# Performance work log

Hardware: AMD Instinct MI355X
Metric: run time of the kernel (lower is better)

The kernel has to match this reference:

```python
import jax, jax.numpy as jnp
import numpy as np

B, N, D, H, C, K = 4096, 64, 128, 256, 8, 3
L = N * D  # latent_dim = num_patches * d_model = 8192
UQ, LQ = 0.9, 0.1


def setup_inputs() -> dict:
    key = jax.random.key(0)
    ks = jax.random.split(key, 6)
    z = jax.random.normal(ks[0], (B, N, D), dtype=jnp.float32)
    q = jax.random.uniform(ks[1], (B,), dtype=jnp.float32)
    ch_ids = jax.random.randint(ks[2], (B,), 0, C, dtype=jnp.int32)
    # Xavier-style init for the 3 expert MLPs (Linear(L,H), Linear(H,L)) + heads Linear(L,1)
    s1 = float(np.sqrt(2.0 / (L + H)))
    s2 = float(np.sqrt(2.0 / (H + L)))
    sh = float(np.sqrt(2.0 / (L + 1)))
    W1 = jax.random.normal(ks[3], (K, L, H), dtype=jnp.float32) * s1
    W2 = jax.random.normal(ks[4], (K, H, L), dtype=jnp.float32) * s2
    Wh = jax.random.normal(ks[5], (K, L), dtype=jnp.float32) * sh
    return dict(z=z, q=q, ch_ids=ch_ids,
                W1=W1, b1=jnp.zeros((K, H), jnp.float32),
                W2=W2, b2=jnp.zeros((K, L), jnp.float32),
                Wh=Wh, bh=jnp.zeros((K,), jnp.float32))


def _channel_thresholds(q, ch_ids):
    """Per-channel sample-adjusted upper/lower quantiles, torch.quantile(..., interpolation='lower')."""
    def one(c):
        mask = ch_ids == c
        n = jnp.sum(mask).astype(jnp.float32)
        s = jnp.sort(jnp.where(mask, q, jnp.inf))  # channel values occupy first n slots
        au = jnp.ceil((n + 1.0) * UQ) / n
        pu = jnp.where(au > 1.0, UQ, au)
        al = jnp.floor((n + 1.0) * LQ) / n
        pl = jnp.where(al < 0.0, LQ, al)
        iu = jnp.floor(pu * (n - 1.0)).astype(jnp.int32)  # 'lower' interpolation index
        il = jnp.floor(pl * (n - 1.0)).astype(jnp.int32)
        return s[iu], s[il]
    return jax.vmap(one)(jnp.arange(C))  # (C,), (C,)


def reference(z, q, ch_ids, W1, b1, W2, b2, Wh, bh):
    uq_th, lq_th = _channel_thresholds(q, ch_ids)
    group = jnp.where(q <= lq_th[ch_ids], 2,
                      jnp.where(q >= uq_th[ch_ids], 0, 1)).astype(jnp.int32)  # (B,)
    zf = z.reshape(z.shape[0], -1)  # (B, L) -- Flatten(start_dim=-2)

    def expert(w1, c1, w2, c2, wh, ch):
        h = jax.nn.gelu(zf @ w1 + c1, approximate=False)   # (B, H)
        o = h @ w2 + c2                                     # (B, L)
        return o @ wh + ch                                  # (B,)

    logits_all = jax.vmap(expert)(W1, b1, W2, b2, Wh, bh)   # (K, B)
    logits = jnp.take_along_axis(logits_all, group[None, :], axis=0)[0]  # (B,)

    # per-channel softmax over logits (stable), matching torch.softmax on each channel's indices
    m = jax.ops.segment_max(logits, ch_ids, num_segments=C)
    e = jnp.exp(logits - m[ch_ids])
    ssum = jax.ops.segment_sum(e, ch_ids, num_segments=C)
    qwa_coeff = e / ssum[ch_ids]
    refined_probs = q * qwa_coeff
    return refined_probs
```

## Files before the change

kernel.cpp:

```cpp
#include <hip/hip_runtime.h>

typedef unsigned short u16;
typedef unsigned int u32;
typedef __attribute__((ext_vector_type(8))) short short8;
typedef __attribute__((ext_vector_type(4))) float f32x4;

#define NB 4096
#define LDIM 8192
#define HDIM 256
#define NEXP 3
#define NCH 8
#define BK 32

__device__ inline u16 f2bf(float f) {
  u32 u = __float_as_uint(f);
  u += 0x7FFFu + ((u >> 16) & 1u);
  return (u16)(u >> 16);
}
__device__ inline u32 pack2(float x, float y) {
  return (u32)f2bf(x) | ((u32)f2bf(y) << 16);
}
__device__ inline void gll16(const void* g, void* l) {
  __builtin_amdgcn_global_load_lds((const __attribute__((address_space(1))) void*)g,
                                   (__attribute__((address_space(3))) void*)l, 16, 0, 0);
}

__global__ void thresh_kernel(const float* __restrict__ q, const int* __restrict__ ch,
                              float* __restrict__ uq_th, float* __restrict__ lq_th) {
  int c = blockIdx.x;
  int tid = threadIdx.x;
  __shared__ float vals[1536];
  __shared__ int oidx[1536];
  __shared__ int n_sh;
  if (tid == 0) n_sh = 0;
  __syncthreads();
  for (int i = tid; i < NB; i += 256) {
    if (ch[i] == c) {
      int p = atomicAdd(&n_sh, 1);
      if (p < 1536) { vals[p] = q[i]; oidx[p] = i; }
    }
  }
  __syncthreads();
  int n = n_sh < 1536 ? n_sh : 1536;
  float nf = (float)n_sh;
  float au = ceilf((nf + 1.0f) * 0.9f) / nf;
  float pu = (au > 1.0f) ? 0.9f : au;
  int iu = (int)floorf(pu * (nf - 1.0f));
  float al = floorf((nf + 1.0f) * 0.1f) / nf;
  float pl = (al < 0.0f) ? 0.1f : al;
  int il = (int)floorf(pl * (nf - 1.0f));
  for (int e = tid; e < n; e += 256) {
    float v = vals[e];
    int oi = oidx[e];
    int r = 0;
    for (int m = 0; m < n; ++m) {
      float vm = vals[m];
      if (vm < v || (vm == v && oidx[m] < oi)) r++;
    }
    if (r == iu) uq_th[c] = v;
    if (r == il) lq_th[c] = v;
  }
}

__global__ void group_kernel(const float* __restrict__ q, const int* __restrict__ ch,
                             const float* __restrict__ uq_th, const float* __restrict__ lq_th,
                             int* __restrict__ group, int* __restrict__ cnt, int* __restrict__ idxl) {
  int b = blockIdx.x * 256 + threadIdx.x;
  if (b >= NB) return;
  float qq = q[b];
  int c = ch[b];
  int g = (qq <= lq_th[c]) ? 2 : ((qq >= uq_th[c]) ? 0 : 1);
  group[b] = g;
  int pos = atomicAdd(&cnt[g], 1);
  idxl[g * NB + pos] = b;
}

__global__ void v_kernel(const float* __restrict__ W2, const float* __restrict__ Wh,
                         float* __restrict__ v) {
  int wv = blockIdx.x * 4 + (threadIdx.x >> 6);
  int lane = threadIdx.x & 63;
  int k = wv >> 8, h = wv & 255;
  const float4* w2 = (const float4*)(W2 + ((size_t)k * HDIM + h) * LDIM);
  const float4* wh = (const float4*)(Wh + (size_t)k * LDIM);
  float s = 0.f;
  for (int i = lane; i < LDIM / 4; i += 64) {
    float4 a = w2[i], b = wh[i];
    s += a.x * b.x + a.y * b.y + a.z * b.z + a.w * b.w;
  }
  for (int off = 32; off; off >>= 1) s += __shfl_down(s, off);
  if (lane == 0) v[k * HDIM + h] = s;
}

__global__ void cbias_kernel(const float* __restrict__ b2, const float* __restrict__ Wh,
                             const float* __restrict__ bh, float* __restrict__ cbias) {
  int k = threadIdx.x >> 6, lane = threadIdx.x & 63;
  float s = 0.f;
  for (int l = lane; l < LDIM; l += 64) s += b2[k * LDIM + l] * Wh[k * LDIM + l];
  for (int off = 32; off; off >>= 1) s += __shfl_down(s, off);
  if (lane == 0) cbias[k] = s + bh[k];
}

__global__ void transpose_kernel(const float* __restrict__ W1, u16* __restrict__ W1t) {
  __shared__ float tile[64][65];
  int k = blockIdx.z;
  int l0 = blockIdx.x * 64;
  int h0 = blockIdx.y * 64;
  int t = threadIdx.x;
  const float* src = W1 + (size_t)k * LDIM * HDIM + (size_t)l0 * HDIM + h0;
  u16* dst = W1t + (size_t)k * HDIM * LDIM + (size_t)h0 * LDIM + l0;
  int hr = t & 63, lr = t >> 6;
#pragma unroll
  for (int p = 0; p < 16; ++p) {
    int l = p * 4 + lr;
    tile[l][hr] = src[(size_t)l * HDIM + hr];
  }
  __syncthreads();
  int cw = t & 7, hw = t >> 3;
#pragma unroll
  for (int p = 0; p < 2; ++p) {
    int h = p * 32 + hw;
    short8 v8;
#pragma unroll
    for (int j = 0; j < 8; ++j) v8[j] = (short)f2bf(tile[cw * 8 + j][h]);
    *(short8*)&dst[(size_t)h * LDIM + cw * 8] = v8;
  }
}

__global__ void __launch_bounds__(256) gemm_kernel(
    const float* __restrict__ z, const u16* __restrict__ W1t,
    const int* __restrict__ idxl, const int* __restrict__ cnt,
    float* __restrict__ part, int nsl, int nt) {
  int zid = blockIdx.z;
  int kexp = zid / nsl, s = zid - kexp * nsl;
  int nk = cnt[kexp];
  int rowbase = blockIdx.x * 64;
  if (rowbase >= nk) return;
  int h0 = blockIdx.y * 64;
  int tid = threadIdx.x;
  int lane = tid & 63, wv = tid >> 6;

  __shared__ __align__(16) u16 As[2][2048];
  __shared__ __align__(16) u16 Bs[2][2048];
  __shared__ int sidx[64];

  const int* idxk = idxl + kexp * NB;
  if (tid < 64) {
    int p = rowbase + tid;
    sidx[tid] = idxk[p < nk ? p : nk - 1];
  }

  int row = tid >> 2, kg = tid & 3;
  int p0 = rowbase + row; if (p0 > nk - 1) p0 = nk - 1;
  int kslice = nt * BK;
  size_t kbase = (size_t)s * kslice;
  const float* zr = z + (size_t)idxk[p0] * LDIM + kbase + kg * 8;
  int sch = kg ^ ((row >> 1) & 3);
  int swA = row * BK + sch * 8;

  const u16* bsrc = W1t + ((size_t)kexp * HDIM + h0 + row) * LDIM + kbase + sch * 8;

  int fr = lane & 15, kgl = (lane >> 4) * 8;
  int kc = kgl >> 3;
  int wr = (wv >> 1) * 32, wc = (wv & 1) * 32;
  int ra0 = wr + fr, ra1 = ra0 + 16, ca0 = wc + fr, ca1 = ca0 + 16;
  int oA0 = ra0 * BK + (kc ^ ((ra0 >> 1) & 3)) * 8;
  int oA1 = ra1 * BK + (kc ^ ((ra1 >> 1) & 3)) * 8;
  int oB0 = ca0 * BK + (kc ^ ((ca0 >> 1) & 3)) * 8;
  int oB1 = ca1 * BK + (kc ^ ((ca1 >> 1) & 3)) * 8;

  f32x4 acc[2][2] = {};
  float4 a0, a1;

  gll16(bsrc, (char*)&Bs[0][0] + wv * 1024);
  a0 = *(const float4*)(zr);
  a1 = *(const float4*)(zr + 4);
  {
    uint4 pa;
    pa.x = pack2(a0.x, a0.y); pa.y = pack2(a0.z, a0.w);
    pa.z = pack2(a1.x, a1.y); pa.w = pack2(a1.z, a1.w);
    *(uint4*)&As[0][swA] = pa;
  }
  __syncthreads();

  int cur = 0;
  for (int t = 0; t < nt; ++t) {
    int nxt = cur ^ 1;
    bool pre = (t + 1 < nt);
    if (pre) {
      int off = (t + 1) * BK;
      gll16(bsrc + off, (char*)&Bs[nxt][0] + wv * 1024);
      a0 = *(const float4*)(zr + off);
      a1 = *(const float4*)(zr + off + 4);
    }
    {
      const u16* Ac = &As[cur][0];
      const u16* Bc = &Bs[cur][0];
      short8 af0 = *(const short8*)&Ac[oA0];
      short8 af1 = *(const short8*)&Ac[oA1];
      short8 bf0 = *(const short8*)&Bc[oB0];
      short8 bf1 = *(const short8*)&Bc[oB1];
      acc[0][0] = __builtin_amdgcn_mfma_f32_16x16x32_bf16(af0, bf0, acc[0][0], 0, 0, 0);
      acc[0][1] = __builtin_amdgcn_mfma_f32_16x16x32_bf16(af0, bf1, acc[0][1], 0, 0, 0);
      acc[1][0] = __builtin_amdgcn_mfma_f32_16x16x32_bf16(af1, bf0, acc[1][0], 0, 0, 0);
      acc[1][1] = __builtin_amdgcn_mfma_f32_16x16x32_bf16(af1, bf1, acc[1][1], 0, 0, 0);
    }
    if (pre) {
      uint4 pa;
      pa.x = pack2(a0.x, a0.y); pa.y = pack2(a0.z, a0.w);
      pa.z = pack2(a1.x, a1.y); pa.w = pack2(a1.z, a1.w);
      *(uint4*)&As[nxt][swA] = pa;
    }
    __syncthreads();
    cur = nxt;
  }

  float* pdst = part + (size_t)s * NB * HDIM;
#pragma unroll
  for (int rb = 0; rb < 2; ++rb)
#pragma unroll
    for (int cb = 0; cb < 2; ++cb)
#pragma unroll
      for (int i = 0; i < 4; ++i) {
        int r = wr + rb * 16 + (lane >> 4) * 4 + i;
        int col = wc + cb * 16 + fr;
        if (rowbase + r < nk)
          pdst[(size_t)sidx[r] * HDIM + h0 + col] = acc[rb][cb][i];
      }
}

__global__ void ep_kernel(const float* __restrict__ part, const float* __restrict__ b1,
                          const float* __restrict__ v, const int* __restrict__ group,
                          float* __restrict__ logits, int nsl) {
  int b = blockIdx.x;
  int t = threadIdx.x;
  int g = group[b];
  size_t o = (size_t)b * HDIM + t;
  const size_t SS = (size_t)NB * HDIM;
  float x = b1[g * HDIM + t];
  for (int i = 0; i < nsl; ++i) x += part[o + i * SS];
  float ge = 0.5f * x * (1.0f + erff(x * 0.70710678118654752f));
  float y = ge * v[g * HDIM + t];
#pragma unroll
  for (int off = 32; off; off >>= 1) y += __shfl_down(y, off);
  __shared__ float red[4];
  int lane = t & 63, wv = t >> 6;
  if (lane == 0) red[wv] = y;
  __syncthreads();
  if (t == 0) logits[b] = red[0] + red[1] + red[2] + red[3];
}

__global__ void softmax_kernel(const float* __restrict__ logits, const float* __restrict__ cbias,
                               const int* __restrict__ group, const float* __restrict__ q,
                               const int* __restrict__ ch, float* __restrict__ out) {
  int c = blockIdx.x;
  int tid = threadIdx.x;
  __shared__ float red[256];
  float m = -3.4e38f;
  for (int i = tid; i < NB; i += 256)
    if (ch[i] == c) {
      float x = logits[i] + cbias[group[i]];
      m = fmaxf(m, x);
    }
  red[tid] = m;
  __syncthreads();
  for (int s = 128; s > 0; s >>= 1) {
    if (tid < s) red[tid] = fmaxf(red[tid], red[tid + s]);
    __syncthreads();
  }
  m = red[0];
  __syncthreads();
  float sum = 0.f;
  for (int i = tid; i < NB; i += 256)
    if (ch[i] == c) sum += expf(logits[i] + cbias[group[i]] - m);
  red[tid] = sum;
  __syncthreads();
  for (int s = 128; s > 0; s >>= 1) {
    if (tid < s) red[tid] += red[tid + s];
    __syncthreads();
  }
  float S = red[0];
  for (int i = tid; i < NB; i += 256)
    if (ch[i] == c) out[i] = q[i] * expf(logits[i] + cbias[group[i]] - m) / S;
}

extern "C" void kernel_launch(void* const* d_in, const int* in_sizes, int n_in,
                              void* d_out, int out_size, void* d_ws, size_t ws_size,
                              hipStream_t stream) {
  const float* z  = (const float*)d_in[0];
  const float* q  = (const float*)d_in[1];
  const int*   ch = (const int*)d_in[2];
  const float* W1 = (const float*)d_in[3];
  const float* b1 = (const float*)d_in[4];
  const float* W2 = (const float*)d_in[5];
  const float* b2 = (const float*)d_in[6];
  const float* Wh = (const float*)d_in[7];
  const float* bh = (const float*)d_in[8];
  float* out = (float*)d_out;

  float* wsf    = (float*)d_ws;
  float* logits = wsf;
  int*   cnt    = (int*)(wsf + 4096);
  float* uq_th  = wsf + 4100;
  float* lq_th  = wsf + 4108;
  float* cbias  = wsf + 4116;
  float* v      = wsf + 4120;
  int*   group  = (int*)(wsf + 4888);
  int*   idxl   = (int*)(wsf + 8984);
  u16*   W1t    = (u16*)(wsf + 21272);
  float* part   = wsf + 3167000;

  size_t need8 = (size_t)3167000 * 4 + (size_t)8 * NB * HDIM * 4;
  int nsl = (ws_size >= need8) ? 8 : 4;
  int nt = (LDIM / nsl) / BK;

  hipMemsetAsync((char*)d_ws + 4096 * 4, 0, 16, stream);
  hipLaunchKernelGGL(thresh_kernel, dim3(NCH), dim3(256), 0, stream, q, ch, uq_th, lq_th);
  hipLaunchKernelGGL(group_kernel, dim3(16), dim3(256), 0, stream, q, ch, uq_th, lq_th, group, cnt, idxl);
  hipLaunchKernelGGL(v_kernel, dim3(192), dim3(256), 0, stream, W2, Wh, v);
  hipLaunchKernelGGL(cbias_kernel, dim3(1), dim3(192), 0, stream, b2, Wh, bh, cbias);
  hipLaunchKernelGGL(transpose_kernel, dim3(128, 4, 3), dim3(256), 0, stream, W1, W1t);
  hipLaunchKernelGGL(gemm_kernel, dim3(64, 4, NEXP * nsl), dim3(256), 0, stream,
                     z, W1t, idxl, cnt, part, nsl, nt);
  hipLaunchKernelGGL(ep_kernel, dim3(NB), dim3(256), 0, stream, part, b1, v, group, logits, nsl);
  hipLaunchKernelGGL(softmax_kernel, dim3(NCH), dim3(256), 0, stream, logits, cbias, group, q, ch, out);
}
```

Baseline: 575.0 us.

## Enlarge GEMM block tile to 128x128 with 4x4 MFMA per wave

Increases the gathered-row GEMM tile from 64x64 to 128x128, so each wave computes a 64x64 sub-tile with 16 MFMAs per K step instead of 4. Each block now loads two A rows and two B rows per thread per step. The aim is better reuse of the z and W1 data staged in LDS and more MFMA work per synchronization. The cost is fewer blocks (halved in each of the M and N grid dimensions), more wasted rows in the partial last tile of each expert, and higher register pressure under launch_bounds(256,2).

```diff
diff --git a/kernel.cpp b/kernel.cpp
--- a/kernel.cpp
+++ b/kernel.cpp
@@ -11,6 +11,8 @@
 #define NEXP 3
 #define NCH 8
 #define BK 32
+#define BM 128
+#define BN 128
 
 __device__ inline u16 f2bf(float f) {
   u32 u = __float_as_uint(f);
@@ -126,59 +128,75 @@
   }
 }
 
-__global__ void __launch_bounds__(256) gemm_kernel(
+__global__ void __launch_bounds__(256, 2) gemm_kernel(
     const float* __restrict__ z, const u16* __restrict__ W1t,
     const int* __restrict__ idxl, const int* __restrict__ cnt,
     float* __restrict__ part, int nsl, int nt) {
   int zid = blockIdx.z;
   int kexp = zid / nsl, s = zid - kexp * nsl;
   int nk = cnt[kexp];
-  int rowbase = blockIdx.x * 64;
+  int rowbase = blockIdx.x * BM;
   if (rowbase >= nk) return;
-  int h0 = blockIdx.y * 64;
+  int h0 = blockIdx.y * BN;
   int tid = threadIdx.x;
   int lane = tid & 63, wv = tid >> 6;
 
-  __shared__ __align__(16) u16 As[2][2048];
-  __shared__ __align__(16) u16 Bs[2][2048];
-  __shared__ int sidx[64];
+  __shared__ __align__(16) u16 As[2][BM * BK];
+  __shared__ __align__(16) u16 Bs[2][BN * BK];
+  __shared__ int sidx[BM];
 
   const int* idxk = idxl + kexp * NB;
-  if (tid < 64) {
+  if (tid < BM) {
     int p = rowbase + tid;
     sidx[tid] = idxk[p < nk ? p : nk - 1];
   }
 
-  int row = tid >> 2, kg = tid & 3;
-  int p0 = rowbase + row; if (p0 > nk - 1) p0 = nk - 1;
   int kslice = nt * BK;
   size_t kbase = (size_t)s * kslice;
-  const float* zr = z + (size_t)idxk[p0] * LDIM + kbase + kg * 8;
-  int sch = kg ^ ((row >> 1) & 3);
-  int swA = row * BK + sch * 8;
-
-  const u16* bsrc = W1t + ((size_t)kexp * HDIM + h0 + row) * LDIM + kbase + sch * 8;
-
-  int fr = lane & 15, kgl = (lane >> 4) * 8;
-  int kc = kgl >> 3;
-  int wr = (wv >> 1) * 32, wc = (wv & 1) * 32;
-  int ra0 = wr + fr, ra1 = ra0 + 16, ca0 = wc + fr, ca1 = ca0 + 16;
-  int oA0 = ra0 * BK + (kc ^ ((ra0 >> 1) & 3)) * 8;
-  int oA1 = ra1 * BK + (kc ^ ((ra1 >> 1) & 3)) * 8;
-  int oB0 = ca0 * BK + (kc ^ ((ca0 >> 1) & 3)) * 8;
-  int oB1 = ca1 * BK + (kc ^ ((ca1 >> 1) & 3)) * 8;
-
-  f32x4 acc[2][2] = {};
-  float4 a0, a1;
-
-  gll16(bsrc, (char*)&Bs[0][0] + wv * 1024);
-  a0 = *(const float4*)(zr);
-  a1 = *(const float4*)(zr + 4);
+
+  int r = tid >> 2, c = tid & 3;
+  int pA0 = rowbase + r;        if (pA0 > nk - 1) pA0 = nk - 1;
+  int pA1 = rowbase + r + 64;   if (pA1 > nk - 1) pA1 = nk - 1;
+  const float* zr0 = z + (size_t)idxk[pA0] * LDIM + kbase + c * 8;
+  const float* zr1 = z + (size_t)idxk[pA1] * LDIM + kbase + c * 8;
+  int swA0 = r * BK + ((c ^ ((r >> 1) & 3)) * 8);
+  int swA1 = (r + 64) * BK + ((c ^ (((r + 64) >> 1) & 3)) * 8);
+
+  int brow0 = wv * 16 + (lane >> 2);
+  int brow1 = brow0 + 64;
+  const u16* bsrc0 = W1t + ((size_t)kexp * HDIM + h0 + brow0) * LDIM + kbase +
+                     (size_t)(((lane & 3) ^ ((brow0 >> 1) & 3)) * 8);
+  const u16* bsrc1 = W1t + ((size_t)kexp * HDIM + h0 + brow1) * LDIM + kbase +
+                     (size_t)(((lane & 3) ^ ((brow1 >> 1) & 3)) * 8);
+
+  int fr = lane & 15, kc = lane >> 4;
+  int wr = (wv >> 1) * 64, wn = (wv & 1) * 64;
+  int oA[4], oB[4];
+#pragma unroll
+  for (int m = 0; m < 4; ++m) {
+    int ra = wr + m * 16 + fr;
+    oA[m] = ra * BK + ((kc ^ ((ra >> 1) & 3)) * 8);
+    int cb = wn + m * 16 + fr;
+    oB[m] = cb * BK + ((kc ^ ((cb >> 1) & 3)) * 8);
+  }
+
+  f32x4 acc[4][4] = {};
+  float4 a00, a01, a10, a11;
+
+  gll16(bsrc0, (char*)&Bs[0][0] + wv * 1024);
+  gll16(bsrc1, (char*)&Bs[0][0] + 4096 + wv * 1024);
+  a00 = *(const float4*)(zr0);
+  a01 = *(const float4*)(zr0 + 4);
+  a10 = *(const float4*)(zr1);
+  a11 = *(const float4*)(zr1 + 4);
   {
-    uint4 pa;
-    pa.x = pack2(a0.x, a0.y); pa.y = pack2(a0.z, a0.w);
-    pa.z = pack2(a1.x, a1.y); pa.w = pack2(a1.z, a1.w);
-    *(uint4*)&As[0][swA] = pa;
+    uint4 p0, p1;
+    p0.x = pack2(a00.x, a00.y); p0.y = pack2(a00.z, a00.w);
+    p0.z = pack2(a01.x, a01.y); p0.w = pack2(a01.z, a01.w);
+    p1.x = pack2(a10.x, a10.y); p1.y = pack2(a10.z, a10.w);
+    p1.z = pack2(a11.x, a11.y); p1.w = pack2(a11.z, a11.w);
+    *(uint4*)&As[0][swA0] = p0;
+    *(uint4*)&As[0][swA1] = p1;
   }
   __syncthreads();
 
@@ -188,27 +206,35 @@
     bool pre = (t + 1 < nt);
     if (pre) {
       int off = (t + 1) * BK;
-      gll16(bsrc + off, (char*)&Bs[nxt][0] + wv * 1024);
-      a0 = *(const float4*)(zr + off);
-      a1 = *(const float4*)(zr + off + 4);
+      gll16(bsrc0 + off, (char*)&Bs[nxt][0] + wv * 1024);
+      gll16(bsrc1 + off, (char*)&Bs[nxt][0] + 4096 + wv * 1024);
+      a00 = *(const float4*)(zr0 + off);
+      a01 = *(const float4*)(zr0 + off + 4);
+      a10 = *(const float4*)(zr1 + off);
+      a11 = *(const float4*)(zr1 + off + 4);
     }
     {
       const u16* Ac = &As[cur][0];
       const u16* Bc = &Bs[cur][0];
-      short8 af0 = *(const short8*)&Ac[oA0];
-      short8 af1 = *(const short8*)&Ac[oA1];
-      short8 bf0 = *(const short8*)&Bc[oB0];
-      short8 bf1 = *(const short8*)&Bc[oB1];
-      acc[0][0] = __builtin_amdgcn_mfma_f32_16x16x32_bf16(af0, bf0, acc[0][0], 0, 0, 0);
-      acc[0][1] = __builtin_amdgcn_mfma_f32_16x16x32_bf16(af0, bf1, acc[0][1], 0, 0, 0);
-      acc[1][0] = __builtin_amdgcn_mfma_f32_16x16x32_bf16(af1, bf0, acc[1][0], 0, 0, 0);
-      acc[1][1] = __builtin_amdgcn_mfma_f32_16x16x32_bf16(af1, bf1, acc[1][1], 0, 0, 0);
+      short8 af[4], bf[4];
+#pragma unroll
+      for (int m = 0; m < 4; ++m) af[m] = *(const short8*)&Ac[oA[m]];
+#pragma unroll
+      for (int n = 0; n < 4; ++n) bf[n] = *(const short8*)&Bc[oB[n]];
+#pragma unroll
+      for (int m = 0; m < 4; ++m)
+#pragma unroll
+        for (int n = 0; n < 4; ++n)
+          acc[m][n] = __builtin_amdgcn_mfma_f32_16x16x32_bf16(af[m], bf[n], acc[m][n], 0, 0, 0);
     }
     if (pre) {
-      uint4 pa;
-      pa.x = pack2(a0.x, a0.y); pa.y = pack2(a0.z, a0.w);
-      pa.z = pack2(a1.x, a1.y); pa.w = pack2(a1.z, a1.w);
-      *(uint4*)&As[nxt][swA] = pa;
+      uint4 p0, p1;
+      p0.x = pack2(a00.x, a00.y); p0.y = pack2(a00.z, a00.w);
+      p0.z = pack2(a01.x, a01.y); p0.w = pack2(a01.z, a01.w);
+      p1.x = pack2(a10.x, a10.y); p1.y = pack2(a10.z, a10.w);
+      p1.z = pack2(a11.x, a11.y); p1.w = pack2(a11.z, a11.w);
+      *(uint4*)&As[nxt][swA0] = p0;
+      *(uint4*)&As[nxt][swA1] = p1;
     }
     __syncthreads();
     cur = nxt;
@@ -216,16 +242,16 @@
 
   float* pdst = part + (size_t)s * NB * HDIM;
 #pragma unroll
-  for (int rb = 0; rb < 2; ++rb)
-#pragma unroll
-    for (int cb = 0; cb < 2; ++cb)
-#pragma unroll
-      for (int i = 0; i < 4; ++i) {
-        int r = wr + rb * 16 + (lane >> 4) * 4 + i;
-        int col = wc + cb * 16 + fr;
-        if (rowbase + r < nk)
-          pdst[(size_t)sidx[r] * HDIM + h0 + col] = acc[rb][cb][i];
+  for (int m = 0; m < 4; ++m)
+#pragma unroll
+    for (int i = 0; i < 4; ++i) {
+      int row = wr + m * 16 + ((lane >> 4) << 2) + i;
+      if (rowbase + row < nk) {
+        float* rp = pdst + (size_t)sidx[row] * HDIM + h0;
+#pragma unroll
+        for (int n = 0; n < 4; ++n) rp[wn + n * 16 + fr] = acc[m][n][i];
       }
+    }
 }
 
 __global__ void ep_kernel(const float* __restrict__ part, const float* __restrict__ b1,
@@ -319,7 +345,7 @@
   hipLaunchKernelGGL(v_kernel, dim3(192), dim3(256), 0, stream, W2, Wh, v);
   hipLaunchKernelGGL(cbias_kernel, dim3(1), dim3(192), 0, stream, b2, Wh, bh, cbias);
   hipLaunchKernelGGL(transpose_kernel, dim3(128, 4, 3), dim3(256), 0, stream, W1, W1t);
-  hipLaunchKernelGGL(gemm_kernel, dim3(64, 4, NEXP * nsl), dim3(256), 0, stream,
+  hipLaunchKernelGGL(gemm_kernel, dim3(NB / BM, HDIM / BN, NEXP * nsl), dim3(256), 0, stream,
                      z, W1t, idxl, cnt, part, nsl, nt);
   hipLaunchKernelGGL(ep_kernel, dim3(NB), dim3(256), 0, stream, part, b1, v, group, logits, nsl);
   hipLaunchKernelGGL(softmax_kernel, dim3(NCH), dim3(256), 0, stream, logits, cbias, group, q, ch, out);
```

Measured after the change: 564.9 us. No clear change (-1.7%).
